# Kernel tuning notes

Measured on AMD Instinct MI355X. Metric: run time of the kernel, lower is better.

The kernel has to match this reference:

```python
import jax, jax.numpy as jnp
import numpy as np

B, L = 16, 1024
D_MODEL, D_STATE, N_LAYERS = 256, 16, 2
FRAME_DIM, N_FRAMES, N_ACT = 115, 4, 19
GNN_H, GNN_K, ACT_EMB, GRID, N_PLAYERS = 32, 6, 16, 5, 22


def _ln(x, g, b, eps=1e-5):
    m = x.mean(-1, keepdims=True)
    v = ((x - m) ** 2).mean(-1, keepdims=True)
    return (x - m) / jnp.sqrt(v + eps) * g + b


def _kan(x, g, b, Wsp, Wbase, bias, beta):
    # x: [N, FRAME_DIM]
    grid = jnp.linspace(-1.0, 1.0, GRID)
    x = _ln(x, g, b)
    bta = jnp.clip(beta, 0.5, 6.0)
    basis = jnp.exp(-((x[..., None] - grid) ** 2) * bta)  # [N, I, G]
    # original: einsum('bdig,oid->bod').sum(-1) with basis dim d==1 broadcast
    # == sum over i, g (basis) and d (spline grid axis)
    spline = jnp.einsum('big,oid->bo', basis, Wsp)
    base = x @ Wbase.T
    return base + spline + bias


def _graph(fc, fp):
    # fc, fp: [N, 115] current / previous frame
    Bn = fc.shape[0]
    ball = fc[:, :2]
    lp = fc[:, 3:25].reshape(Bn, 11, 2)
    rp = fc[:, 25:47].reshape(Bn, 11, 2)
    lpp = fp[:, 3:25].reshape(Bn, 11, 2)
    rpp = fp[:, 25:47].reshape(Bn, 11, 2)
    pos = jnp.concatenate([lp, rp], 1)           # [N, 22, 2]
    posp = jnp.concatenate([lpp, rpp], 1)
    vel = pos - posp
    team = jnp.concatenate([jnp.zeros((Bn, 11, 1)), jnp.ones((Bn, 11, 1))], 1)
    bd = jnp.sqrt(((pos - ball[:, None, :]) ** 2).sum(-1, keepdims=True))
    prox = jnp.exp(-bd * 2)
    lc = lp.mean(1, keepdims=True)
    rc = rp.mean(1, keepdims=True)
    tc = jnp.concatenate([jnp.broadcast_to(lc, (Bn, 11, 2)),
                          jnp.broadcast_to(rc, (Bn, 11, 2))], 1)
    nodes = jnp.concatenate([pos, vel, team, prox, pos - tc], -1)  # [N, 22, 8]
    eye = jnp.eye(N_PLAYERS)
    d = jnp.sqrt(((pos[:, :, None, :] - pos[:, None, :, :]) ** 2).sum(-1)) + eye * 1e6
    _, idx = jax.lax.top_k(-d, GNN_K)
    adj = jax.nn.one_hot(idx, N_PLAYERS).sum(-2)
    adj = jnp.minimum(adj + eye, 1.0)
    adj = adj / jnp.clip(adj.sum(-1, keepdims=True), 1.0, None)
    # the torch model computes the graph under no_grad
    return jax.lax.stop_gradient(nodes), jax.lax.stop_gradient(adj)


def _s6(x, h0, lng, lnb, Win, Wdt, bdt, Alog, WB, WC, Dp, Wout):
    Bn, Ln, Dm = x.shape
    h0 = h0.reshape(Bn, Dm, D_STATE)
    xn = _ln(x, lng, lnb)
    xz = xn @ Win.T
    x_in, z = jnp.split(xz, 2, axis=-1)
    dt = jax.nn.softplus(x_in @ Wdt.T + bdt)     # [B, L, D]
    A = -jnp.exp(Alog)                            # [D, N]
    Bt = x_in @ WB.T                              # [B, L, N]
    Ct = x_in @ WC.T

    def step(h, inp):
        dt_t, x_t, B_t, C_t = inp                 # [B,D],[B,D],[B,N],[B,N]
        dA = jnp.exp(dt_t[:, :, None] * A)        # [B, D, N]
        h = dA * h + (dt_t * x_t)[:, :, None] * B_t[:, None, :]
        y = (h * C_t[:, None, :]).sum(-1)         # [B, D]
        return h, y

    hL, ys = jax.lax.scan(step, h0, (dt.swapaxes(0, 1), x_in.swapaxes(0, 1),
                                     Bt.swapaxes(0, 1), Ct.swapaxes(0, 1)))
    y = ys.swapaxes(0, 1)
    ssm = y * jax.nn.silu(z) + x_in * Dp
    return x + ssm @ Wout.T, hL.reshape(Bn, -1)


def setup_inputs() -> dict:
    key = jax.random.key(0)
    ks = iter(jax.random.split(key, 80))

    def nrm(shape, s=0.05):
        return jax.random.normal(next(ks), shape, dtype=jnp.float32) * s

    inp = {}
    inp['obs'] = jax.random.normal(next(ks), (B, L, N_FRAMES, FRAME_DIM), dtype=jnp.float32)
    inp['prev_actions'] = jax.random.randint(next(ks), (B, L), 0, N_ACT)
    inp['h0_0'] = jnp.zeros((B, D_MODEL * D_STATE), jnp.float32)
    inp['h0_1'] = jnp.zeros((B, D_MODEL * D_STATE), jnp.float32)
    inp['kan_ln_g'] = jnp.ones((FRAME_DIM,), jnp.float32)
    inp['kan_ln_b'] = jnp.zeros((FRAME_DIM,), jnp.float32)
    inp['kan_spline'] = nrm((D_MODEL, FRAME_DIM, GRID), 0.1)
    inp['kan_scale'] = jnp.ones((D_MODEL, FRAME_DIM), jnp.float32)
    inp['kan_bias'] = jnp.zeros((D_MODEL,), jnp.float32)
    inp['kan_beta'] = jnp.full((1,), 2.0, jnp.float32)
    inp['fn_g'] = jnp.ones((D_MODEL,), jnp.float32)
    inp['fn_b'] = jnp.zeros((D_MODEL,), jnp.float32)
    inp['gnn_W'] = nrm((GNN_H, 8))
    inp['edge_w'] = jnp.full((1,), 0.5, jnp.float32)
    inp['act_emb'] = nrm((N_ACT, ACT_EMB), 1.0)
    inp['W_ip'] = nrm((D_MODEL, D_MODEL + GNN_H + ACT_EMB))
    inp['b_ip'] = jnp.zeros((D_MODEL,), jnp.float32)
    for i in range(N_LAYERS):
        p = 'm%d_' % i
        inp[p + 'lng'] = jnp.ones((D_MODEL,), jnp.float32)
        inp[p + 'lnb'] = jnp.zeros((D_MODEL,), jnp.float32)
        inp[p + 'Win'] = nrm((2 * D_MODEL, D_MODEL))
        inp[p + 'Wdt'] = nrm((D_MODEL, D_MODEL))
        inp[p + 'bdt'] = jnp.zeros((D_MODEL,), jnp.float32)
        inp[p + 'Alog'] = jax.random.uniform(next(ks), (D_MODEL, D_STATE),
                                             minval=-3.0, maxval=-1.0, dtype=jnp.float32)
        inp[p + 'WB'] = nrm((D_STATE, D_MODEL))
        inp[p + 'WC'] = nrm((D_STATE, D_MODEL))
        inp[p + 'D'] = jnp.ones((D_MODEL,), jnp.float32)
        inp[p + 'Wout'] = nrm((D_MODEL, D_MODEL))
    inp['fl_g'] = jnp.ones((D_MODEL,), jnp.float32)
    inp['fl_b'] = jnp.zeros((D_MODEL,), jnp.float32)
    inp['pW1'] = nrm((128, D_MODEL)); inp['pb1'] = jnp.zeros((128,), jnp.float32)
    inp['pW2'] = nrm((N_ACT, 128)); inp['pb2'] = jnp.zeros((N_ACT,), jnp.float32)
    inp['vW1'] = nrm((64, D_MODEL)); inp['vb1'] = jnp.zeros((64,), jnp.float32)
    inp['vW2'] = nrm((1, 64)); inp['vb2'] = jnp.zeros((1,), jnp.float32)
    return inp


def reference(obs, prev_actions, h0_0, h0_1,
              kan_ln_g, kan_ln_b, kan_spline, kan_scale, kan_bias, kan_beta,
              fn_g, fn_b, gnn_W, edge_w, act_emb, W_ip, b_ip,
              m0_lng, m0_lnb, m0_Win, m0_Wdt, m0_bdt, m0_Alog, m0_WB, m0_WC, m0_D, m0_Wout,
              m1_lng, m1_lnb, m1_Win, m1_Wdt, m1_bdt, m1_Alog, m1_WB, m1_WC, m1_D, m1_Wout,
              fl_g, fl_b, pW1, pb1, pW2, pb2, vW1, vb1, vW2, vb2):
    BL = B * L
    # frame encoder (KAN) over all frames of all timesteps
    flat = obs.reshape(BL * N_FRAMES, FRAME_DIM)
    fe = _kan(flat, kan_ln_g, kan_ln_b, kan_spline, kan_scale, kan_bias, kan_beta)
    fe = jax.nn.relu(_ln(fe.reshape(BL, N_FRAMES, D_MODEL), fn_g, fn_b))
    feat = fe.mean(1)                                   # [BL, D]
    # GNN on last two frames
    fc = obs[:, :, -1, :].reshape(BL, FRAME_DIM)
    fp = obs[:, :, -2, :].reshape(BL, FRAME_DIM)
    nodes, adj = _graph(fc, fp)
    gx = nodes @ gnn_W.T                                # [BL, 22, H]
    agg = jnp.einsum('bij,bjd->bid', adj, gx)
    gx = gx * (1 - edge_w) + agg * edge_w
    gemb = gx.mean(1)                                   # [BL, H]
    aemb = act_emb[prev_actions].reshape(BL, ACT_EMB)
    x = jnp.concatenate([feat, gemb, aemb], -1) @ W_ip.T + b_ip
    x = x.reshape(B, L, D_MODEL)
    x, h1 = _s6(x, h0_0, m0_lng, m0_lnb, m0_Win, m0_Wdt, m0_bdt, m0_Alog, m0_WB, m0_WC, m0_D, m0_Wout)
    x, h2 = _s6(x, h0_1, m1_lng, m1_lnb, m1_Win, m1_Wdt, m1_bdt, m1_Alog, m1_WB, m1_WC, m1_D, m1_Wout)
    x = _ln(x, fl_g, fl_b)
    logits = jax.nn.relu(x @ pW1.T + pb1) @ pW2.T + pb2   # [B, L, N_ACT]
    value = (jax.nn.relu(x @ vW1.T + vb1) @ vW2.T + vb2)[..., 0]  # [B, L]
    return logits, value, h1, h2
```

## Files before the change

### kernel.cpp

```cpp
#include <hip/hip_runtime.h>
#include <math.h>

#define BB   16
#define LL   1024
#define BLR  (BB*LL)
#define DM   256
#define DS   16
#define FD   115
#define NF   4
#define NACTN 19
#define GH   32
#define GKN  6
#define AEM  16
#define NP   22
#define CATD 304
#define CATP 320
#define KKANP 256
#define KREALK 230
#define NC   16
#define CL   (LL/NC)
#define TT   16
#define XZW  800


typedef __attribute__((ext_vector_type(8))) short bf16x8;
typedef __attribute__((ext_vector_type(4))) float f32x4;

__device__ inline unsigned short f2bf(float f) {
    unsigned int u = __float_as_uint(f);
    u += 0x7fff + ((u >> 16) & 1);
    return (unsigned short)(u >> 16);
}
__device__ inline unsigned int f2bf2(float lo, float hi) {
    return (unsigned int)f2bf(lo) | ((unsigned int)f2bf(hi) << 16);
}
__device__ inline size_t swz(int row, int k) {
    return (size_t)(row >> 4)*4096 + (k >> 5)*512 + ((k >> 3) & 3)*128
         + (row & 15)*8 + (k & 7);
}
__device__ inline size_t swz320(int row, int k) {
    return (size_t)(row >> 4)*5120 + (k >> 5)*512 + ((k >> 3) & 3)*128
         + (row & 15)*8 + (k & 7);
}

template<int NFRAG, int KFRAG>
__global__ __launch_bounds__(256) void bgemm(
    const unsigned short* __restrict__ A, const unsigned short* __restrict__ W,
    const float* __restrict__ bias, float* __restrict__ C,
    int ldc, int act, int accum)
{
    const int tid = threadIdx.x;
    const int wid = tid >> 6, lane = tid & 63;
    const int wr = wid >> 1, wc = wid & 1;
    const int g = lane >> 4, r16 = lane & 15;
    const int bm = blockIdx.x * 64;
    const int bn = blockIdx.y * (NFRAG * 32);
    const int RB = KFRAG * 512;

    f32x4 acc[2][NFRAG] = {};
    const unsigned short* abase = A + ((size_t)(bm >> 4) + wr*2)*RB + g*128 + r16*8;
    const unsigned short* wbase = W + ((size_t)(bn >> 4) + wc*NFRAG)*RB + g*128 + r16*8;
    #pragma unroll
    for (int kk = 0; kk < KFRAG; ++kk) {
        bf16x8 a0 = *(const bf16x8*)(abase + kk*512);
        bf16x8 a1 = *(const bf16x8*)(abase + RB + kk*512);
        bf16x8 bfr[NFRAG];
        #pragma unroll
        for (int ni = 0; ni < NFRAG; ++ni)
            bfr[ni] = *(const bf16x8*)(wbase + (size_t)ni*RB + kk*512);
        #pragma unroll
        for (int ni = 0; ni < NFRAG; ++ni) {
            acc[0][ni] = __builtin_amdgcn_mfma_f32_16x16x32_bf16(a0, bfr[ni], acc[0][ni], 0,0,0);
            acc[1][ni] = __builtin_amdgcn_mfma_f32_16x16x32_bf16(a1, bfr[ni], acc[1][ni], 0,0,0);
        }
    }
    #pragma unroll
    for (int mi = 0; mi < 2; ++mi) {
        #pragma unroll
        for (int j = 0; j < 4; ++j) {
            int row = bm + wr*32 + mi*16 + g*4 + j;
            float* crow = C + (size_t)row * ldc;
            #pragma unroll
            for (int ni = 0; ni < NFRAG; ++ni) {
                int col = bn + wc*(NFRAG*16) + ni*16 + r16;
                float v = acc[mi][ni][j];
                if (act == 3) {
                    if (col >= 512 && col < 768) {
                        v += bias[col - 512];
                        v = fmaxf(v, 0.f) + __logf(1.f + __expf(-fabsf(v)));
                    }
                } else {
                    if (bias) v += bias[col];
                    if (act == 1) v = fmaxf(v, 0.f);
                }
                if (accum) v += crow[col];
                crow[col] = v;
            }
        }
    }
}

__global__ __launch_bounds__(256) void bgemm_ln(
    const unsigned short* __restrict__ A, const unsigned short* __restrict__ W,
    float* __restrict__ X, const float* __restrict__ g8p,
    const float* __restrict__ b8p, unsigned short* __restrict__ Y16)
{
    __shared__ float rsum[64][2];
    __shared__ float rsq[64][2];
    const int tid = threadIdx.x;
    const int bm = blockIdx.x * 64;
    const int wid = tid >> 6, lane = tid & 63;
    const int wr = wid >> 1, wc = wid & 1;
    const int g = lane >> 4, r16 = lane & 15;

    f32x4 acc[2][8] = {};
    const unsigned short* abase = A + ((size_t)(bm >> 4) + wr*2)*4096 + g*128 + r16*8;
    const unsigned short* wbase = W + (size_t)(wc*8)*4096 + g*128 + r16*8;
    #pragma unroll
    for (int kk = 0; kk < 8; ++kk) {
        bf16x8 a0 = *(const bf16x8*)(abase + kk*512);
        bf16x8 a1 = *(const bf16x8*)(abase + 4096 + kk*512);
        bf16x8 bfr[8];
        #pragma unroll
        for (int ni = 0; ni < 8; ++ni)
            bfr[ni] = *(const bf16x8*)(wbase + (size_t)ni*4096 + kk*512);
        #pragma unroll
        for (int ni = 0; ni < 8; ++ni) {
            acc[0][ni] = __builtin_amdgcn_mfma_f32_16x16x32_bf16(a0, bfr[ni], acc[0][ni], 0,0,0);
            acc[1][ni] = __builtin_amdgcn_mfma_f32_16x16x32_bf16(a1, bfr[ni], acc[1][ni], 0,0,0);
        }
    }
    #pragma unroll
    for (int mi = 0; mi < 2; ++mi) {
        #pragma unroll
        for (int j = 0; j < 4; ++j) {
            int row = bm + wr*32 + mi*16 + g*4 + j;
            float* xrow = X + (size_t)row * DM;
            float s = 0.f, q = 0.f;
            #pragma unroll
            for (int ni = 0; ni < 8; ++ni) {
                int col = wc*128 + ni*16 + r16;
                float v = acc[mi][ni][j] + xrow[col];
                acc[mi][ni][j] = v;
                xrow[col] = v;
                s += v; q += v*v;
            }
            #pragma unroll
            for (int off = 1; off < 16; off <<= 1) {
                s += __shfl_xor(s, off);
                q += __shfl_xor(q, off);
            }
            if (r16 == 0) {
                int lrow = wr*32 + mi*16 + g*4 + j;
                rsum[lrow][wc] = s; rsq[lrow][wc] = q;
            }
        }
    }
    __syncthreads();
    float g8[8], b8[8];
    #pragma unroll
    for (int ni = 0; ni < 8; ++ni) {
        int col = wc*128 + ni*16 + r16;
        g8[ni] = g8p[col]; b8[ni] = b8p[col];
    }
    #pragma unroll
    for (int mi = 0; mi < 2; ++mi) {
        #pragma unroll
        for (int j = 0; j < 4; ++j) {
            int lrow = wr*32 + mi*16 + g*4 + j;
            int row = bm + lrow;
            float sm = rsum[lrow][0] + rsum[lrow][1];
            float sq = rsq[lrow][0] + rsq[lrow][1];
            float mn = sm * (1.f/256.f);
            float var = fmaxf(sq * (1.f/256.f) - mn*mn, 0.f);
            float rstd = rsqrtf(var + 1e-5f);
            #pragma unroll
            for (int ni = 0; ni < 8; ++ni) {
                int col = wc*128 + ni*16 + r16;
                float v = (acc[mi][ni][j] - mn) * rstd * g8[ni] + b8[ni];
                Y16[swz(row, col)] = f2bf(v);
            }
        }
    }
}

__global__ __launch_bounds__(256) void kan_statgen(
    const float* __restrict__ obs, const float* __restrict__ lng,
    const float* __restrict__ lnb, const float* __restrict__ betap,
    unsigned short* __restrict__ AG)
{
    int row = blockIdx.x * 4 + (threadIdx.x >> 6);
    int l = threadIdx.x & 63;
    const float beta = fminf(fmaxf(betap[0], 0.5f), 6.0f);
    const float* o = obs + (size_t)row * FD;
    float v0 = o[l];
    float v1 = (l + 64 < FD) ? o[l + 64] : 0.f;
    float s = v0 + v1;
    for (int off = 32; off; off >>= 1) s += __shfl_xor(s, off);
    float m = s * (1.f / FD);
    float e0 = v0 - m;
    float e1 = (l + 64 < FD) ? (v1 - m) : 0.f;
    float ss = e0*e0 + e1*e1;
    for (int off = 32; off; off >>= 1) ss += __shfl_xor(ss, off);
    float rs = rsqrtf(ss * (1.f / FD) + 1e-5f);

    float x0 = e0 * rs * lng[l] + lnb[l];
    float sb0 = 0.f;
    #pragma unroll
    for (int g5 = 0; g5 < 5; ++g5) {
        float dx = x0 - (-1.f + 0.5f * (float)g5);
        sb0 += __expf(-dx*dx*beta);
    }
    unsigned int u0 = f2bf2(x0, sb0);
    unsigned int u1 = 0u;
    if (l + 64 < FD) {
        float x1 = e1 * rs * lng[l+64] + lnb[l+64];
        float sb1 = 0.f;
        #pragma unroll
        for (int g5 = 0; g5 < 5; ++g5) {
            float dx = x1 - (-1.f + 0.5f * (float)g5);
            sb1 += __expf(-dx*dx*beta);
        }
        u1 = f2bf2(x1, sb1);
    }
    size_t base = (size_t)(row >> 4) * 4096 + (row & 15) * 8
                + ((l >> 2) & 3) * 128 + ((2*l) & 7);
    *(unsigned int*)(AG + base + ((l >> 4)    ) * 512) = u0;
    *(unsigned int*)(AG + base + ((l >> 4) + 4) * 512) = u1;
}

__global__ void prep_kanw(const float* __restrict__ sp, const float* __restrict__ sc,
                          const float* __restrict__ W_ip,
                          unsigned short* __restrict__ WF16,
                          unsigned short* __restrict__ WIP320)
{
    int idx = blockIdx.x * 256 + threadIdx.x;
    if (idx < DM*KKANP) {
        int o = idx >> 8, k = idx & 255;
        float v = 0.f;
        if (k < KREALK) {
            int i = k >> 1;
            if (k & 1) {
                const float* s5 = sp + ((size_t)o*FD + i)*5;
                v = s5[0] + s5[1] + s5[2] + s5[3] + s5[4];
            } else v = sc[o*FD + i];
        }
        WF16[swz(o, k)] = f2bf(v);
    } else if (idx < DM*KKANP + DM*CATP) {
        int j = idx - DM*KKANP;
        int o = j / CATP, k = j - o * CATP;
        float v = (k < CATD) ? W_ip[(size_t)o*CATD + k] : 0.f;
        WIP320[swz320(o, k)] = f2bf(v);
    }
}

__global__ __launch_bounds__(256) void kan_gemm2(
    const unsigned short* __restrict__ AG, const unsigned short* __restrict__ WF,
    const float* __restrict__ kbias, const float* __restrict__ fng,
    const float* __restrict__ fnb, unsigned short* __restrict__ CAT16)
{
    __shared__ float rsum[64][2];
    __shared__ float rsq[64][2];
    const int tid = threadIdx.x;
    const int bm = blockIdx.x * 64;
    const int wid = tid >> 6, lane = tid & 63;
    const int wr = wid >> 1, wc = wid & 1;
    const int g = lane >> 4, r16 = lane & 15;

    f32x4 acc[2][8] = {};
    const unsigned short* abase = AG + ((size_t)(bm >> 4) + wr*2)*4096 + g*128 + r16*8;
    const unsigned short* wbase = WF + (size_t)(wc*8)*4096 + g*128 + r16*8;
    #pragma unroll
    for (int kk = 0; kk < 8; ++kk) {
        bf16x8 af0 = *(const bf16x8*)(abase + kk*512);
        bf16x8 af1 = *(const bf16x8*)(abase + 4096 + kk*512);
        bf16x8 bfr[8];
        #pragma unroll
        for (int ni = 0; ni < 8; ++ni)
            bfr[ni] = *(const bf16x8*)(wbase + (size_t)ni*4096 + kk*512);
        #pragma unroll
        for (int ni = 0; ni < 8; ++ni) {
            acc[0][ni] = __builtin_amdgcn_mfma_f32_16x16x32_bf16(af0, bfr[ni], acc[0][ni], 0,0,0);
            acc[1][ni] = __builtin_amdgcn_mfma_f32_16x16x32_bf16(af1, bfr[ni], acc[1][ni], 0,0,0);
        }
    }
    float bias8[8], g8[8], b8[8];
    #pragma unroll
    for (int ni = 0; ni < 8; ++ni) {
        int col = wc*128 + ni*16 + r16;
        bias8[ni] = kbias[col]; g8[ni] = fng[col]; b8[ni] = fnb[col];
    }
    #pragma unroll
    for (int mi = 0; mi < 2; ++mi) {
        #pragma unroll
        for (int j = 0; j < 4; ++j) {
            float s = 0.f, q = 0.f;
            #pragma unroll
            for (int ni = 0; ni < 8; ++ni) {
                float v = acc[mi][ni][j] + bias8[ni];
                s += v; q += v*v;
            }
            #pragma unroll
            for (int off = 1; off < 16; off <<= 1) {
                s += __shfl_xor(s, off);
                q += __shfl_xor(q, off);
            }
            if (r16 == 0) {
                int row = wr*32 + mi*16 + g*4 + j;
                rsum[row][wc] = s; rsq[row][wc] = q;
            }
        }
    }
    __syncthreads();
    #pragma unroll
    for (int mi = 0; mi < 2; ++mi) {
        int row0 = wr*32 + mi*16 + g*4;
        float o8[8] = {0.f,0.f,0.f,0.f,0.f,0.f,0.f,0.f};
        #pragma unroll
        for (int j = 0; j < 4; ++j) {
            int row = row0 + j;
            float sm = rsum[row][0] + rsum[row][1];
            float sq = rsq[row][0] + rsq[row][1];
            float mn = sm * (1.f/256.f);
            float var = fmaxf(sq * (1.f/256.f) - mn*mn, 0.f);
            float rstd = rsqrtf(var + 1e-5f);
            #pragma unroll
            for (int ni = 0; ni < 8; ++ni) {
                float v = acc[mi][ni][j] + bias8[ni];
                v = (v - mn) * rstd * g8[ni] + b8[ni];
                o8[ni] += fmaxf(v, 0.f);
            }
        }
        int rbl = (bm + row0) >> 2;
        #pragma unroll
        for (int ni = 0; ni < 8; ++ni)
            CAT16[swz320(rbl, wc*128 + ni*16 + r16)] = f2bf(o8[ni] * 0.25f);
    }
}

__global__ __launch_bounds__(256) void gemm_f32(
    const float* __restrict__ A, const float* __restrict__ W,
    const float* __restrict__ bias, float* __restrict__ C,
    int N, int K, int lda, int ldc, int act, int accum)
{
    __shared__ float As[16][68];
    __shared__ float Ws[16][68];
    const int tid = threadIdx.x;
    const int bm = blockIdx.x * 64;
    const int bn = blockIdx.y * 64;
    const int ty = tid >> 4, tx = tid & 15;
    const int lr = tid >> 2;
    const int lk = (tid & 3) * 4;
    float acc[4][4] = {{0.f,0.f,0.f,0.f},{0.f,0.f,0.f,0.f},{0.f,0.f,0.f,0.f},{0.f,0.f,0.f,0.f}};

    for (int k0 = 0; k0 < K; k0 += 16) {
        float4 av = *reinterpret_cast<const float4*>(A + (size_t)(bm + lr) * lda + k0 + lk);
        As[lk+0][lr] = av.x; As[lk+1][lr] = av.y; As[lk+2][lr] = av.z; As[lk+3][lr] = av.w;
        float4 wv = make_float4(0.f, 0.f, 0.f, 0.f);
        if (bn + lr < N)
            wv = *reinterpret_cast<const float4*>(W + (size_t)(bn + lr) * K + k0 + lk);
        Ws[lk+0][lr] = wv.x; Ws[lk+1][lr] = wv.y; Ws[lk+2][lr] = wv.z; Ws[lk+3][lr] = wv.w;
        __syncthreads();
        #pragma unroll
        for (int kk = 0; kk < 16; ++kk) {
            float4 a4 = *reinterpret_cast<const float4*>(&As[kk][ty*4]);
            float4 b4 = *reinterpret_cast<const float4*>(&Ws[kk][tx*4]);
            float aa[4] = {a4.x, a4.y, a4.z, a4.w};
            float bb[4] = {b4.x, b4.y, b4.z, b4.w};
            #pragma unroll
            for (int i = 0; i < 4; ++i)
                #pragma unroll
                for (int j = 0; j < 4; ++j)
                    acc[i][j] = fmaf(aa[i], bb[j], acc[i][j]);
        }
        __syncthreads();
    }
    #pragma unroll
    for (int i = 0; i < 4; ++i) {
        int row = bm + ty*4 + i;
        #pragma unroll
        for (int j = 0; j < 4; ++j) {
            int col = bn + tx*4 + j;
            if (col < N) {
                float v = acc[i][j];
                if (bias) v += bias[col];
                if (act == 1) v = fmaxf(v, 0.f);
                size_t o = (size_t)row * ldc + col;
                if (accum) v += C[o];
                C[o] = v;
            }
        }
    }
}

__global__ void prep_layerw2(
    const float* __restrict__ Win0, const float* __restrict__ WB0,
    const float* __restrict__ WC0, const float* __restrict__ Wdt0,
    const float* __restrict__ Wout0,
    const float* __restrict__ Win1, const float* __restrict__ WB1,
    const float* __restrict__ WC1, const float* __restrict__ Wdt1,
    const float* __restrict__ Wout1,
    const float* __restrict__ pW1, const float* __restrict__ vW1,
    const float* __restrict__ pb1, const float* __restrict__ vb1,
    unsigned short* __restrict__ WX0, unsigned short* __restrict__ WO0,
    unsigned short* __restrict__ WX1, unsigned short* __restrict__ WO1,
    unsigned short* __restrict__ PV16, float* __restrict__ PVB)
{
    int idx = blockIdx.x * 256 + threadIdx.x;
    int ly = blockIdx.y;
    if (ly == 2) {
        if (idx < 192*256) {
            int n = idx >> 8, k = idx & 255;
            float v = (n < 128) ? pW1[(size_t)n*DM + k] : vW1[(size_t)(n-128)*DM + k];
            PV16[swz(n, k)] = f2bf(v);
        } else if (idx < 192*256 + 192) {
            int i = idx - 192*256;
            PVB[i] = (i < 128) ? pb1[i] : vb1[i-128];
        }
        return;
    }
    const float* Win  = ly ? Win1 : Win0;
    const float* WB   = ly ? WB1  : WB0;
    const float* WC   = ly ? WC1  : WC0;
    const float* Wdt  = ly ? Wdt1 : Wdt0;
    const float* Wout = ly ? Wout1 : Wout0;
    unsigned short* WINX16 = ly ? WX1 : WX0;
    unsigned short* WOUT16 = ly ? WO1 : WO0;
    if (idx < 512*256) {
        int n = idx >> 8, k = idx & 255;
        WINX16[swz(n, k)] = f2bf(Win[idx]);
    } else if (idx < 768*256) {
        int j2 = idx - 512*256;
        int n = j2 >> 8, k = j2 & 255;
        const float* src = Wdt + (size_t)n*DM;
        float acc = 0.f;
        for (int j = 0; j < DM; ++j)
            acc = fmaf(src[j], Win[(size_t)j*DM + k], acc);
        WINX16[swz(512 + n, k)] = f2bf(acc);
    } else if (idx < 800*256) {
        int j2 = idx - 768*256;
        int n = j2 >> 8, k = j2 & 255;
        const float* src = (n < 16) ? (WB + n*DM) : (WC + (n-16)*DM);
        float acc = 0.f;
        for (int j = 0; j < DM; ++j)
            acc = fmaf(src[j], Win[(size_t)j*DM + k], acc);
        WINX16[swz(768 + n, k)] = f2bf(acc);
    } else if (idx < 800*256 + 256*256) {
        int j2 = idx - 800*256;
        int n = j2 >> 8, k = j2 & 255;
        WOUT16[swz(n, k)] = f2bf(Wout[j2]);
    }
}

__global__ __launch_bounds__(64) void graph_kernel(const float* __restrict__ obs,
    const float* __restrict__ gW, const float* __restrict__ ewp,
    unsigned short* __restrict__ CAT16)
{
    __shared__ float px[NP], py[NP];
    __shared__ float nodes[NP][8];
    __shared__ float gxs[NP][GH];
    __shared__ unsigned int msk[NP];
    __shared__ float rden[NP];
    __shared__ float wgt[NP];
    const int row = blockIdx.x;
    const int lane = threadIdx.x;
    const float* fc = obs + ((size_t)row * NF + 3) * FD;
    const float* fp = obs + ((size_t)row * NF + 2) * FD;
    const float ew = ewp[0];

    if (lane < NP) {
        int i = lane;
        float p0, p1, q0, q1;
        if (i < 11) { p0 = fc[3+2*i];  p1 = fc[4+2*i];  q0 = fp[3+2*i];  q1 = fp[4+2*i]; }
        else { int ii = i-11; p0 = fc[25+2*ii]; p1 = fc[26+2*ii]; q0 = fp[25+2*ii]; q1 = fp[26+2*ii]; }
        px[i] = p0; py[i] = p1;
        float bx = fc[0], by = fc[1];
        float bd = sqrtf((p0-bx)*(p0-bx) + (p1-by)*(p1-by));
        nodes[i][0] = p0; nodes[i][1] = p1;
        nodes[i][2] = p0 - q0; nodes[i][3] = p1 - q1;
        nodes[i][4] = (i < 11) ? 0.f : 1.f;
        nodes[i][5] = __expf(-2.f * bd);
    }
    __syncthreads();
    if (lane < NP) {
        int base = (lane < 11) ? 0 : 11;
        float cx = 0.f, cy = 0.f;
        for (int j = 0; j < 11; ++j) { cx += px[base+j]; cy += py[base+j]; }
        cx *= (1.f/11.f); cy *= (1.f/11.f);
        nodes[lane][6] = px[lane] - cx;
        nodes[lane][7] = py[lane] - cy;
        unsigned sel = 0;
        for (int k = 0; k < GKN; ++k) {
            float best = 1e30f; int bj = 0;
            for (int j = 0; j < NP; ++j) {
                if (j == lane || ((sel >> j) & 1u)) continue;
                float dx = px[lane]-px[j], dy = py[lane]-py[j];
                float dd = sqrtf(dx*dx + dy*dy);
                if (dd < best) { best = dd; bj = j; }
            }
            sel |= (1u << bj);
        }
        unsigned full = sel | (1u << lane);
        msk[lane] = full;
        rden[lane] = 1.f / fmaxf((float)__popc(full), 1.f);
    }
    __syncthreads();
    for (int idx = lane; idx < NP*GH; idx += 64) {
        int i = idx >> 5, h = idx & 31;
        float s = 0.f;
        #pragma unroll
        for (int f = 0; f < 8; ++f) s += nodes[i][f] * gW[h*8 + f];
        gxs[i][h] = s;
    }
    __syncthreads();
    if (lane < NP) {
        float s = 0.f;
        for (int i = 0; i < NP; ++i) if ((msk[i] >> lane) & 1u) s += rden[i];
        wgt[lane] = (1.f - ew) + ew * s;
    }
    __syncthreads();
    if (lane < GH) {
        float s = 0.f;
        for (int j = 0; j < NP; ++j) s += wgt[j] * gxs[j][lane];
        CAT16[swz320(row, DM + lane)] = f2bf(s * (1.f/22.f));
    }
}

__global__ void gather_aemb32(const int* __restrict__ pa, const float* __restrict__ emb,
                              unsigned short* __restrict__ CAT16)
{
    int idx = blockIdx.x * 256 + threadIdx.x;
    int row = idx >> 5, e = idx & 31;
    float v = (e < AEM) ? emb[pa[row]*AEM + e] : 0.f;
    CAT16[swz320(row, DM + GH + e)] = f2bf(v);
}

__global__ __launch_bounds__(256) void ln256_swz(const float* __restrict__ X,
    const float* __restrict__ g, const float* __restrict__ b,
    unsigned short* __restrict__ Y16)
{
    int row = blockIdx.x * 4 + (threadIdx.x >> 6);
    int lane = threadIdx.x & 63;
    const float* x = X + (size_t)row * DM;
    float4 v = reinterpret_cast<const float4*>(x)[lane];
    float s = v.x + v.y + v.z + v.w;
    for (int off = 32; off; off >>= 1) s += __shfl_xor(s, off);
    float m = s * (1.f / DM);
    float d0 = v.x-m, d1 = v.y-m, d2 = v.z-m, d3 = v.w-m;
    float ss = d0*d0 + d1*d1 + d2*d2 + d3*d3;
    for (int off = 32; off; off >>= 1) ss += __shfl_xor(ss, off);
    float rstd = rsqrtf(ss * (1.f / DM) + 1e-5f);
    int c = lane * 4;
    float o0 = d0*rstd*g[c+0] + b[c+0];
    float o1 = d1*rstd*g[c+1] + b[c+1];
    float o2 = d2*rstd*g[c+2] + b[c+2];
    float o3 = d3*rstd*g[c+3] + b[c+3];
    size_t base = swz(row, c);
    *(uint2*)(Y16 + base) = make_uint2(f2bf2(o0, o1), f2bf2(o2, o3));
}

__global__ __launch_bounds__(256) void s6_chunkA(
    const float* __restrict__ xz, const float* __restrict__ Alog,
    float* __restrict__ P, float* __restrict__ S)
{
    __shared__ float sdt[TT][64], sx[TT][64];
    __shared__ __align__(16) float sB[TT][16];
    const int blk = blockIdx.x;
    const int dblk = blk & 3, c = (blk >> 2) & 15, b = blk >> 6;
    const int sg = threadIdx.x & 3, dl = threadIdx.x >> 2;
    const int d0 = dblk*64, d = d0 + dl;
    float A[4];
    #pragma unroll
    for (int k = 0; k < 4; ++k) A[k] = -__expf(Alog[d*DS + sg*4 + k]);
    const size_t r0 = (size_t)b*LL + c*CL;
    const int lt = threadIdx.x >> 4, lc = (threadIdx.x & 15) * 4;
    float Pv[4] = {1.f,1.f,1.f,1.f}, Sv[4] = {0.f,0.f,0.f,0.f};
    for (int t0 = 0; t0 < CL; t0 += TT) {
        size_t rb = r0 + t0 + lt;
        *(float4*)&sdt[lt][lc] = *(const float4*)(xz + rb*XZW + 512 + d0 + lc);
        *(float4*)&sx[lt][lc]  = *(const float4*)(xz + rb*XZW + d0 + lc);
        if (threadIdx.x < 64) {
            size_t rb2 = r0 + t0 + (threadIdx.x >> 2);
            *(float4*)&sB[threadIdx.x >> 2][(threadIdx.x & 3)*4] =
                *(const float4*)(xz + rb2*XZW + 768 + (threadIdx.x & 3)*4);
        }
        __syncthreads();
        #pragma unroll
        for (int tt = 0; tt < TT; ++tt) {
            float dtv = sdt[tt][dl];
            float u   = dtv * sx[tt][dl];
            float4 Bv = *(const float4*)&sB[tt][sg*4];
            float bb[4] = {Bv.x, Bv.y, Bv.z, Bv.w};
            #pragma unroll
            for (int k = 0; k < 4; ++k) {
                float dA = __expf(dtv * A[k]);
                Pv[k] *= dA;
                Sv[k] = fmaf(dA, Sv[k], u * bb[k]);
            }
        }
        __syncthreads();
    }
    size_t o = (((size_t)b*NC + c)*DM + d)*DS + sg*4;
    *(float4*)(P + o) = make_float4(Pv[0], Pv[1], Pv[2], Pv[3]);
    *(float4*)(S + o) = make_float4(Sv[0], Sv[1], Sv[2], Sv[3]);
}

__global__ __launch_bounds__(256) void s6_comb(
    const float* __restrict__ P, const float* __restrict__ S,
    const float* __restrict__ h0, float* __restrict__ hin, float* __restrict__ hout)
{
    int idx = blockIdx.x * 256 + threadIdx.x;
    int b = idx >> 12, ds = idx & 4095;
    float h = h0[idx];
    #pragma unroll
    for (int c = 0; c < NC; ++c) {
        size_t o = (((size_t)b*NC + c) << 12) + ds;
        hin[o] = h;
        h = fmaf(P[o], h, S[o]);
    }
    hout[idx] = h;
}

__global__ __launch_bounds__(256) void s6_chunkC(
    const float* __restrict__ xz, const float* __restrict__ Alog,
    const float* __restrict__ hin, const float* __restrict__ Dp,
    unsigned short* __restrict__ ssm16)
{
    __shared__ float sdt[TT][64], sx[TT][64], sz[TT][64];
    __shared__ __align__(16) float sB[TT][16], sC[TT][16];
    const int blk = blockIdx.x;
    const int dblk = blk & 3, c = (blk >> 2) & 15, b = blk >> 6;
    const int sg = threadIdx.x & 3, dl = threadIdx.x >> 2;
    const int d0 = dblk*64, d = d0 + dl;
    float A[4];
    #pragma unroll
    for (int k = 0; k < 4; ++k) A[k] = -__expf(Alog[d*DS + sg*4 + k]);
    const float Dv = Dp[d];
    const size_t r0 = (size_t)b*LL + c*CL;
    const int lt = threadIdx.x >> 4, lc = (threadIdx.x & 15) * 4;
    float4 h4 = *(const float4*)(hin + (((size_t)b*NC + c)*DM + d)*DS + sg*4);
    float h[4] = {h4.x, h4.y, h4.z, h4.w};
    for (int t0 = 0; t0 < CL; t0 += TT) {
        size_t rb = r0 + t0 + lt;
        *(float4*)&sdt[lt][lc] = *(const float4*)(xz + rb*XZW + 512 + d0 + lc);
        *(float4*)&sx[lt][lc]  = *(const float4*)(xz + rb*XZW + d0 + lc);
        *(float4*)&sz[lt][lc]  = *(const float4*)(xz + rb*XZW + 256 + d0 + lc);
        if (threadIdx.x < 128) {
            size_t rb2 = r0 + t0 + ((threadIdx.x & 63) >> 2);
            int col = (threadIdx.x & 3) * 4;
            if (threadIdx.x < 64)
                *(float4*)&sB[(threadIdx.x & 63) >> 2][col] =
                    *(const float4*)(xz + rb2*XZW + 768 + col);
            else
                *(float4*)&sC[(threadIdx.x & 63) >> 2][col] =
                    *(const float4*)(xz + rb2*XZW + 784 + col);
        }
        __syncthreads();
        #pragma unroll
        for (int tt = 0; tt < TT; ++tt) {
            float dtv = sdt[tt][dl];
            float xv  = sx[tt][dl];
            float u   = dtv * xv;
            float4 Bv = *(const float4*)&sB[tt][sg*4];
            float4 Cv = *(const float4*)&sC[tt][sg*4];
            float bb[4] = {Bv.x, Bv.y, Bv.z, Bv.w};
            float cc[4] = {Cv.x, Cv.y, Cv.z, Cv.w};
            float p = 0.f;
            #pragma unroll
            for (int k = 0; k < 4; ++k) {
                float dA = __expf(dtv * A[k]);
                h[k] = fmaf(dA, h[k], u * bb[k]);
                p = fmaf(h[k], cc[k], p);
            }
            p += __shfl_xor(p, 1);
            p += __shfl_xor(p, 2);
            if (sg == 0) {
                float zv = sz[tt][dl];
                float sil = zv / (1.f + __expf(-zv));
                int row = (int)(r0 + t0 + tt);
                ssm16[swz(row, d)] = f2bf(fmaf(p, sil, xv * Dv));
            }
        }
        __syncthreads();
    }
}

static inline void gemm(hipStream_t st, const float* A, const float* W, const float* bias,
                        float* C, int M, int N, int K, int lda, int ldc, int act, int accum) {
    dim3 g(M/64, (N+63)/64);
    gemm_f32<<<g, 256, 0, st>>>(A, W, bias, C, N, K, lda, ldc, act, accum);
}

extern "C" void kernel_launch(void* const* d_in, const int* in_sizes, int n_in,
                              void* d_out, int out_size, void* d_ws, size_t ws_size,
                              hipStream_t stream) {
    (void)in_sizes; (void)n_in; (void)out_size; (void)ws_size;
    const float* obs      = (const float*)d_in[0];
    const int*   pa       = (const int*)d_in[1];
    const float* h0in[2]  = {(const float*)d_in[2], (const float*)d_in[3]};
    const float* kan_ln_g = (const float*)d_in[4];
    const float* kan_ln_b = (const float*)d_in[5];
    const float* kan_sp   = (const float*)d_in[6];
    const float* kan_sc   = (const float*)d_in[7];
    const float* kan_bias = (const float*)d_in[8];
    const float* kan_beta = (const float*)d_in[9];
    const float* fn_g     = (const float*)d_in[10];
    const float* fn_b     = (const float*)d_in[11];
    const float* gnn_W    = (const float*)d_in[12];
    const float* edge_w   = (const float*)d_in[13];
    const float* act_emb  = (const float*)d_in[14];
    const float* W_ip     = (const float*)d_in[15];
    const float* b_ip     = (const float*)d_in[16];
    const float* fl_g     = (const float*)d_in[37];
    const float* fl_b     = (const float*)d_in[38];
    const float* pW1      = (const float*)d_in[39];
    const float* pb1      = (const float*)d_in[40];
    const float* pW2      = (const float*)d_in[41];
    const float* pb2      = (const float*)d_in[42];
    const float* vW1      = (const float*)d_in[43];
    const float* vb1      = (const float*)d_in[44];
    const float* vW2      = (const float*)d_in[45];
    const float* vb2      = (const float*)d_in[46];

    const size_t SZ_BIG = (size_t)BLR * DM;
    float* ws = (float*)d_ws;
    float* X    = ws;
    float* R0   = X + SZ_BIG;
    unsigned short* XN16  = (unsigned short*)R0;
    unsigned short* SSM16 = XN16 + (size_t)BLR*DM;
    unsigned short* WF16   = (unsigned short*)R0;
    unsigned short* WIP320 = WF16 + (size_t)DM*KKANP;
    float* XZBC = R0 + SZ_BIG;
    unsigned short* AG16 = (unsigned short*)XZBC;
    float* R4   = XZBC + (size_t)BLR * XZW;
    unsigned short* CAT16 = (unsigned short*)R4;
    const size_t CH = (size_t)BB * NC * DM * DS;
    float* Pbuf = R4;
    float* Sbuf = R4 + CH;
    float* HIN  = R4 + 2*CH;
    unsigned short* WINX16[2];
    WINX16[0] = (unsigned short*)(R4 + 3*CH);
    WINX16[1] = WINX16[0] + (size_t)XZW*DM;
    unsigned short* WOUT16[2];
    WOUT16[0] = WINX16[1] + (size_t)XZW*DM;
    WOUT16[1] = WOUT16[0] + DM*DM;
    unsigned short* PV16 = WOUT16[1] + DM*DM;
    float* PVB = (float*)(PV16 + 192*DM);

    float* out        = (float*)d_out;
    float* out_logits = out;
    float* out_value  = out + (size_t)BLR * NACTN;
    float* out_h[2]   = {out + (size_t)BLR*NACTN + BLR,
                         out + (size_t)BLR*NACTN + BLR + (size_t)BB*DM*DS};

    prep_kanw<<<(DM*KKANP + DM*CATP + 255)/256, 256, 0, stream>>>(
        kan_sp, kan_sc, W_ip, WF16, WIP320);
    kan_statgen<<<BLR*NF/4, 256, 0, stream>>>(obs, kan_ln_g, kan_ln_b, kan_beta, AG16);
    kan_gemm2<<<BLR*NF/64, 256, 0, stream>>>(AG16, WF16, kan_bias, fn_g, fn_b, CAT16);
    graph_kernel<<<BLR, 64, 0, stream>>>(obs, gnn_W, edge_w, CAT16);
    gather_aemb32<<<BLR*32/256, 256, 0, stream>>>(pa, act_emb, CAT16);

    bgemm<8,10><<<dim3(BLR/64, 1), 256, 0, stream>>>(CAT16, WIP320, b_ip, X, DM, 0, 0);

    prep_layerw2<<<dim3((800*256 + 256*256 + 255)/256, 3), 256, 0, stream>>>(
        (const float*)d_in[19], (const float*)d_in[23], (const float*)d_in[24],
        (const float*)d_in[20], (const float*)d_in[26],
        (const float*)d_in[29], (const float*)d_in[33], (const float*)d_in[34],
        (const float*)d_in[30], (const float*)d_in[36],
        pW1, vW1, pb1, vb1,
        WINX16[0], WOUT16[0], WINX16[1], WOUT16[1], PV16, PVB);

    ln256_swz<<<BLR/4, 256, 0, stream>>>(X, (const float*)d_in[17], (const float*)d_in[18], XN16);

    for (int l = 0; l < 2; ++l) {
        const float* bdt  = (const float*)d_in[17 + 10*l + 4];
        const float* Alog = (const float*)d_in[17 + 10*l + 5];
        const float* Dp   = (const float*)d_in[17 + 10*l + 8];
        const float* nlg  = (l == 0) ? (const float*)d_in[27] : fl_g;
        const float* nlb  = (l == 0) ? (const float*)d_in[28] : fl_b;

        bgemm<5,8><<<dim3(BLR/64, 5), 256, 0, stream>>>(
            XN16, WINX16[l], bdt, XZBC, XZW, 3, 0);
        s6_chunkA<<<BB*NC*4, 256, 0, stream>>>(XZBC, Alog, Pbuf, Sbuf);
        s6_comb<<<BB*DM*DS/256, 256, 0, stream>>>(Pbuf, Sbuf, h0in[l], HIN, out_h[l]);
        s6_chunkC<<<BB*NC*4, 256, 0, stream>>>(XZBC, Alog, HIN, Dp, SSM16);
        bgemm_ln<<<BLR/64, 256, 0, stream>>>(SSM16, WOUT16[l], X, nlg, nlb, XN16);
    }

    float* H = XZBC;
    bgemm<6,8><<<dim3(BLR/64, 1), 256, 0, stream>>>(XN16, PV16, PVB, H, 192, 1, 0);
    gemm(stream, H, pW2, pb2, out_logits, BLR, NACTN, 128, 192, NACTN, 0, 0);
    gemm(stream, H + 128, vW2, vb2, out_value, BLR, 1, 64, 192, 1, 0, 0);
}
```

Measured before the change: 353.5 us.

## Parallelize graph kNN via rank counting and fuse action-embedding gather into graph kernel

Replaces the per-lane serial 6-pass nearest-neighbour selection (22 of 64 lanes each computing 6x22 distances) with a shared-memory distance matrix computed by all 64 lanes, followed by a parallel rank count that marks the six closest neighbours per node. Ties break on lower index, matching the earlier first-found rule. It also folds the action-embedding gather into idle lanes of the graph kernel, which removes one kernel launch. The cost is extra shared memory and two more barriers per block.

```diff
diff --git a/kernel.cpp b/kernel.cpp
--- a/kernel.cpp
+++ b/kernel.cpp
@@ -454,10 +454,13 @@
 
 __global__ __launch_bounds__(64) void graph_kernel(const float* __restrict__ obs,
     const float* __restrict__ gW, const float* __restrict__ ewp,
+    const int* __restrict__ pa, const float* __restrict__ emb,
     unsigned short* __restrict__ CAT16)
 {
     __shared__ float px[NP], py[NP];
     __shared__ float nodes[NP][8];
+    __shared__ float sdist[NP][NP+1];
+    __shared__ unsigned int sflag[NP][NP+1];
     __shared__ float gxs[NP][GH];
     __shared__ unsigned int msk[NP];
     __shared__ float rden[NP];
@@ -480,6 +483,10 @@
         nodes[i][2] = p0 - q0; nodes[i][3] = p1 - q1;
         nodes[i][4] = (i < 11) ? 0.f : 1.f;
         nodes[i][5] = __expf(-2.f * bd);
+    } else if (lane >= 32) {
+        int e = lane - 32;
+        float v = (e < AEM) ? emb[pa[row]*AEM + e] : 0.f;
+        CAT16[swz320(row, DM + GH + e)] = f2bf(v);
     }
     __syncthreads();
     if (lane < NP) {
@@ -489,17 +496,32 @@
         cx *= (1.f/11.f); cy *= (1.f/11.f);
         nodes[lane][6] = px[lane] - cx;
         nodes[lane][7] = py[lane] - cy;
+    }
+    for (int idx = lane; idx < NP*NP; idx += 64) {
+        int i = idx / NP, j = idx - i*NP;
+        float dd = 1e30f;
+        if (i != j) {
+            float dx = px[i]-px[j], dy = py[i]-py[j];
+            dd = sqrtf(dx*dx + dy*dy);
+        }
+        sdist[i][j] = dd;
+    }
+    __syncthreads();
+    for (int idx = lane; idx < NP*NP; idx += 64) {
+        int i = idx / NP, j = idx - i*NP;
+        float dj = sdist[i][j];
+        int rank = 0;
+        #pragma unroll
+        for (int q = 0; q < NP; ++q) {
+            float dq = sdist[i][q];
+            rank += (dq < dj || (dq == dj && q < j)) ? 1 : 0;
+        }
+        sflag[i][j] = (i != j && rank < GKN) ? 1u : 0u;
+    }
+    __syncthreads();
+    if (lane < NP) {
         unsigned sel = 0;
-        for (int k = 0; k < GKN; ++k) {
-            float best = 1e30f; int bj = 0;
-            for (int j = 0; j < NP; ++j) {
-                if (j == lane || ((sel >> j) & 1u)) continue;
-                float dx = px[lane]-px[j], dy = py[lane]-py[j];
-                float dd = sqrtf(dx*dx + dy*dy);
-                if (dd < best) { best = dd; bj = j; }
-            }
-            sel |= (1u << bj);
-        }
+        for (int j = 0; j < NP; ++j) sel |= sflag[lane][j] << j;
         unsigned full = sel | (1u << lane);
         msk[lane] = full;
         rden[lane] = 1.f / fmaxf((float)__popc(full), 1.f);
@@ -524,15 +546,6 @@
         for (int j = 0; j < NP; ++j) s += wgt[j] * gxs[j][lane];
         CAT16[swz320(row, DM + lane)] = f2bf(s * (1.f/22.f));
     }
-}
-
-__global__ void gather_aemb32(const int* __restrict__ pa, const float* __restrict__ emb,
-                              unsigned short* __restrict__ CAT16)
-{
-    int idx = blockIdx.x * 256 + threadIdx.x;
-    int row = idx >> 5, e = idx & 31;
-    float v = (e < AEM) ? emb[pa[row]*AEM + e] : 0.f;
-    CAT16[swz320(row, DM + GH + e)] = f2bf(v);
 }
 
 __global__ __launch_bounds__(256) void ln256_swz(const float* __restrict__ X,
@@ -757,8 +770,7 @@
         kan_sp, kan_sc, W_ip, WF16, WIP320);
     kan_statgen<<<BLR*NF/4, 256, 0, stream>>>(obs, kan_ln_g, kan_ln_b, kan_beta, AG16);
     kan_gemm2<<<BLR*NF/64, 256, 0, stream>>>(AG16, WF16, kan_bias, fn_g, fn_b, CAT16);
-    graph_kernel<<<BLR, 64, 0, stream>>>(obs, gnn_W, edge_w, CAT16);
-    gather_aemb32<<<BLR*32/256, 256, 0, stream>>>(pa, act_emb, CAT16);
+    graph_kernel<<<BLR, 64, 0, stream>>>(obs, gnn_W, edge_w, pa, act_emb, CAT16);
 
     bgemm<8,10><<<dim3(BLR/64, 1), 256, 0, stream>>>(CAT16, WIP320, b_ip, X, DM, 0, 0);
 
```

New measurement: 365.6 us. 3.4% more time.
